# Performance work log

Measured on AMD Instinct MI355X. Metric: run time of the kernel, lower is better.

Reference implementation:

```python
import jax, jax.numpy as jnp
import numpy as np

B, T, C, L, H, OD = 8, 1024, 512, 6, 8, 768
DH = C // H
EPS = 1e-5


def _ln(x, w, b):
    mu = jnp.mean(x, axis=-1, keepdims=True)
    var = jnp.mean((x - mu) ** 2, axis=-1, keepdims=True)
    return (x - mu) * jax.lax.rsqrt(var + EPS) * w + b


def setup_inputs() -> dict:
    key = jax.random.key(0)
    ks = jax.random.split(key, 10)
    s = 0.02
    return {
        "observations": jax.random.normal(ks[0], (B, T, OD), jnp.float32),
        "obs_W": jax.random.normal(ks[1], (OD, C), jnp.float32) * s,
        "obs_b": jnp.zeros((C,), jnp.float32),
        "pos_emb": jax.random.normal(ks[2], (1, T + 1, C), jnp.float32) * s,
        "ln1_w": jnp.ones((L, C), jnp.float32),
        "ln1_b": jnp.zeros((L, C), jnp.float32),
        "Wq": jax.random.normal(ks[3], (L, C, C), jnp.float32) * s,
        "bq": jnp.zeros((L, C), jnp.float32),
        "Wk": jax.random.normal(ks[4], (L, C, C), jnp.float32) * s,
        "bk": jnp.zeros((L, C), jnp.float32),
        "Wv": jax.random.normal(ks[5], (L, C, C), jnp.float32) * s,
        "bv": jnp.zeros((L, C), jnp.float32),
        "Wo": jax.random.normal(ks[6], (L, C, C), jnp.float32) * s,
        "bo": jnp.zeros((L, C), jnp.float32),
        "ln2_w": jnp.ones((L, C), jnp.float32),
        "ln2_b": jnp.zeros((L, C), jnp.float32),
        "W1": jax.random.normal(ks[7], (L, C, 4 * C), jnp.float32) * s,
        "b1": jnp.zeros((L, 4 * C), jnp.float32),
        "W2": jax.random.normal(ks[8], (L, 4 * C, C), jnp.float32) * s,
        "b2": jnp.zeros((L, C), jnp.float32),
        "lnf_w": jnp.ones((C,), jnp.float32),
        "lnf_b": jnp.zeros((C,), jnp.float32),
    }


def reference(observations, obs_W, obs_b, pos_emb, ln1_w, ln1_b, Wq, bq, Wk, bk,
              Wv, bv, Wo, bo, ln2_w, ln2_b, W1, b1, W2, b2, lnf_w, lnf_b):
    # obs embedding: Linear + exact GELU
    tok = jax.nn.gelu(observations @ obs_W + obs_b, approximate=False)
    x = tok + pos_emb[:, :T, :]  # past_length = 0
    causal = jnp.tril(jnp.ones((T, T), bool))  # [T,T]
    scale = 1.0 / np.sqrt(DH)
    for i in range(L):
        h = _ln(x, ln1_w[i], ln1_b[i])
        q = (h @ Wq[i] + bq[i]).reshape(B, T, H, DH)
        k = (h @ Wk[i] + bk[i]).reshape(B, T, H, DH)
        v = (h @ Wv[i] + bv[i]).reshape(B, T, H, DH)
        att = jnp.einsum("bqhd,bkhd->bhqk", q, k) * scale
        att = jnp.where(causal, att, -jnp.inf)
        att = jax.nn.softmax(att, axis=-1)
        y = jnp.einsum("bhqk,bkhd->bqhd", att, v).reshape(B, T, C)
        x = x + y @ Wo[i] + bo[i]
        m = _ln(x, ln2_w[i], ln2_b[i])
        m = jax.nn.gelu(m @ W1[i] + b1[i], approximate=False)
        x = x + m @ W2[i] + b2[i]
    return _ln(x, lnf_w, lnf_b)
```

## Files before the change

kernel.cpp:

```cpp
#include <hip/hip_runtime.h>

#define DEVI __device__ __forceinline__

typedef __attribute__((ext_vector_type(8))) short short8;
typedef __attribute__((ext_vector_type(4))) short sh4;
typedef __attribute__((ext_vector_type(4))) float f32x4;

constexpr int Bn = 8, Tn = 1024, Cn = 512, Hn = 8, DHn = 64, Ln = 6, ODn = 768;
constexpr int Mn = Bn * Tn;
constexpr int SQk = 1536;

DEVI short f2bs(float f) {
  unsigned u = __builtin_bit_cast(unsigned, f);
  unsigned r = (u + 0x7FFFu + ((u >> 16) & 1u)) >> 16;
  return (short)r;
}

DEVI float gelu_f(float v) {
  return 0.5f * v * (1.0f + erff(v * 0.70710678118654752f));
}

DEVI void gload_lds16(const void* gp, void* lp) {
  __builtin_amdgcn_global_load_lds(
      (const __attribute__((address_space(1))) unsigned*)gp,
      (__attribute__((address_space(3))) unsigned*)lp, 16, 0, 0);
}

DEVI short8 ld8(const short* p) {
  sh4 a = *(const sh4*)p;
  sh4 b = *(const sh4*)(p + 4);
  return __builtin_shufflevector(a, b, 0, 1, 2, 3, 4, 5, 6, 7);
}

__global__ __launch_bounds__(256) void wtrans4_kernel(
    const float* __restrict__ Wq, const float* __restrict__ Wk,
    const float* __restrict__ Wv, const float* __restrict__ Wo,
    short* __restrict__ wqkvT, short* __restrict__ woT) {
  const int z = blockIdx.z, i = z >> 2, which = z & 3;
  const size_t WCC = (size_t)Cn * Cn;
  const float* W = (which == 0) ? Wq : (which == 1) ? Wk : (which == 2) ? Wv : Wo;
  W += (size_t)i * WCC;
  short* dst = (which < 3) ? (wqkvT + (size_t)i * 3 * WCC + (size_t)which * WCC)
                           : (woT + (size_t)i * WCC);
  __shared__ float tile[32][33];
  const int tx = threadIdx.x & 31, ty = threadIdx.x >> 5;
  const int k0 = blockIdx.y * 32, n0 = blockIdx.x * 32;
#pragma unroll
  for (int q = 0; q < 4; ++q)
    tile[ty + q * 8][tx] = W[(size_t)(k0 + ty + q * 8) * Cn + n0 + tx];
  __syncthreads();
#pragma unroll
  for (int q = 0; q < 4; ++q)
    dst[(size_t)(n0 + ty + q * 8) * Cn + k0 + tx] = f2bs(tile[tx][ty + q * 8]);
}

__global__ __launch_bounds__(256) void wtransL_kernel(
    const float* __restrict__ W, short* __restrict__ Wt, int K, int N) {
  const int l = blockIdx.z;
  W += (size_t)l * K * N;
  Wt += (size_t)l * K * N;
  __shared__ float tile[32][33];
  const int tx = threadIdx.x & 31, ty = threadIdx.x >> 5;
  const int k0 = blockIdx.y * 32, n0 = blockIdx.x * 32;
#pragma unroll
  for (int q = 0; q < 4; ++q)
    tile[ty + q * 8][tx] = W[(size_t)(k0 + ty + q * 8) * N + n0 + tx];
  __syncthreads();
#pragma unroll
  for (int q = 0; q < 4; ++q)
    Wt[(size_t)(n0 + ty + q * 8) * K + k0 + tx] = f2bs(tile[tx][ty + q * 8]);
}

__global__ __launch_bounds__(256) void bcat_kernel(
    const float* __restrict__ bq, const float* __restrict__ bk,
    const float* __restrict__ bv, float* __restrict__ bqkv) {
  const int i = blockIdx.x * 256 + threadIdx.x;
  const int l = i / 1536, c = i - l * 1536;
  float v = (c < 512) ? bq[l * 512 + c]
                      : (c < 1024) ? bk[l * 512 + c - 512] : bv[l * 512 + c - 1024];
  bqkv[i] = v;
}

__global__ __launch_bounds__(256) void cast_kernel(
    const float* __restrict__ in, short* __restrict__ out) {
  const int i = blockIdx.x * 256 + threadIdx.x;
  out[i] = f2bs(in[i]);
}

template <typename OUTT>
__global__ __launch_bounds__(256) void ln_kernel(
    const float* __restrict__ x, const float* __restrict__ w,
    const float* __restrict__ bb, OUTT* __restrict__ out) {
  const int row = blockIdx.x, tid = threadIdx.x;
  const float* xr = x + (size_t)row * Cn;
  const float v0 = xr[tid], v1 = xr[tid + 256];
  float s = v0 + v1, s2 = v0 * v0 + v1 * v1;
#pragma unroll
  for (int m = 1; m < 64; m <<= 1) {
    s += __shfl_xor(s, m);
    s2 += __shfl_xor(s2, m);
  }
  __shared__ float red[8];
  const int wave = tid >> 6, lane = tid & 63;
  if (lane == 0) { red[wave] = s; red[4 + wave] = s2; }
  __syncthreads();
  s = red[0] + red[1] + red[2] + red[3];
  s2 = red[4] + red[5] + red[6] + red[7];
  const float mu = s * (1.0f / Cn);
  const float var = s2 * (1.0f / Cn) - mu * mu;
  const float rstd = rsqrtf(var + 1e-5f);
  const float o0 = (v0 - mu) * rstd * w[tid] + bb[tid];
  const float o1 = (v1 - mu) * rstd * w[tid + 256] + bb[tid + 256];
  if constexpr (sizeof(OUTT) == 2) {
    out[(size_t)row * Cn + tid] = f2bs(o0);
    out[(size_t)row * Cn + tid + 256] = f2bs(o1);
  } else {
    out[(size_t)row * Cn + tid] = o0;
    out[(size_t)row * Cn + tid + 256] = o1;
  }
}

template <int NP, typename OUTT, bool WRITEX>
__global__ __launch_bounds__(256) void lnred_kernel(
    float* __restrict__ x, const float* __restrict__ part,
    const float* __restrict__ w, const float* __restrict__ bb,
    OUTT* __restrict__ out) {
  const int row = blockIdx.x, tid = threadIdx.x;
  const size_t base = (size_t)row * Cn;
  float v0 = x[base + tid], v1 = x[base + tid + 256];
#pragma unroll
  for (int p = 0; p < NP; ++p) {
    v0 += part[(size_t)p * Mn * Cn + base + tid];
    v1 += part[(size_t)p * Mn * Cn + base + tid + 256];
  }
  if constexpr (WRITEX) {
    x[base + tid] = v0;
    x[base + tid + 256] = v1;
  }
  float s = v0 + v1, s2 = v0 * v0 + v1 * v1;
#pragma unroll
  for (int m = 1; m < 64; m <<= 1) {
    s += __shfl_xor(s, m);
    s2 += __shfl_xor(s2, m);
  }
  __shared__ float red[8];
  const int wave = tid >> 6, lane = tid & 63;
  if (lane == 0) { red[wave] = s; red[4 + wave] = s2; }
  __syncthreads();
  s = red[0] + red[1] + red[2] + red[3];
  s2 = red[4] + red[5] + red[6] + red[7];
  const float mu = s * (1.0f / Cn);
  const float var = s2 * (1.0f / Cn) - mu * mu;
  const float rstd = rsqrtf(var + 1e-5f);
  const float o0 = (v0 - mu) * rstd * w[tid] + bb[tid];
  const float o1 = (v1 - mu) * rstd * w[tid + 256] + bb[tid + 256];
  if constexpr (sizeof(OUTT) == 2) {
    out[base + tid] = f2bs(o0);
    out[base + tid + 256] = f2bs(o1);
  } else {
    out[base + tid] = o0;
    out[base + tid + 256] = o1;
  }
}

template <int EPI, int KS>
__global__ __launch_bounds__(256) void gemm_kernel(
    const short* __restrict__ A, const short* __restrict__ Bt,
    const float* __restrict__ bias, short* __restrict__ outb,
    float* __restrict__ resid, const float* __restrict__ pos, int K, int N) {
  __shared__ __align__(16) short As[128 * 64];
  __shared__ __align__(16) short Bs[128 * 64];
  const int tid = threadIdx.x;
  const int lane = tid & 63;
  const int wave = tid >> 6;
  const int m0 = blockIdx.y * 128;
  const int n0 = blockIdx.x * 128;
  const int z = (KS > 1) ? blockIdx.z : 0;
  const int Ksl = K / KS;
  const int wr = (wave >> 1) * 64;
  const int wc = (wave & 1) * 64;
  const int lA = lane & 15;
  const int lg = lane >> 4;

  f32x4 acc[4][4];
#pragma unroll
  for (int a = 0; a < 4; ++a)
#pragma unroll
    for (int b = 0; b < 4; ++b) acc[a][b] = f32x4{0.f, 0.f, 0.f, 0.f};

  const int rS = tid >> 3;
  const int cS = (((tid & 7) ^ ((tid >> 3) & 7))) * 8;
  const short* Ag = A + (size_t)(m0 + rS) * K + cS;
  const short* Bg = Bt + (size_t)(n0 + rS) * K + cS;

  for (int kk = z * Ksl; kk < z * Ksl + Ksl; kk += 64) {
#pragma unroll
    for (int it = 0; it < 4; ++it) {
      gload_lds16(Ag + (size_t)it * 32 * K + kk, &As[it * 2048 + wave * 512]);
      gload_lds16(Bg + (size_t)it * 32 * K + kk, &Bs[it * 2048 + wave * 512]);
    }
    __syncthreads();
#pragma unroll
    for (int ks = 0; ks < 2; ++ks) {
      const int gA = ((ks * 4 + lg) ^ (lA & 7)) * 8;
      short8 af[4], bf[4];
#pragma unroll
      for (int i = 0; i < 4; ++i) {
        af[i] = *(const short8*)&As[(wr + i * 16 + lA) * 64 + gA];
        bf[i] = *(const short8*)&Bs[(wc + i * 16 + lA) * 64 + gA];
      }
#pragma unroll
      for (int mi = 0; mi < 4; ++mi)
#pragma unroll
        for (int ni = 0; ni < 4; ++ni)
          acc[mi][ni] = __builtin_amdgcn_mfma_f32_16x16x32_bf16(
              af[mi], bf[ni], acc[mi][ni], 0, 0, 0);
    }
    __syncthreads();
  }

#pragma unroll
  for (int mi = 0; mi < 4; ++mi) {
    const int row = m0 + wr + mi * 16 + (lane >> 4) * 4;
#pragma unroll
    for (int ni = 0; ni < 4; ++ni) {
      const int col = n0 + wc + ni * 16 + (lane & 15);
      const float bv = (KS == 1 || z == 0) ? bias[col] : 0.f;
#pragma unroll
      for (int j = 0; j < 4; ++j) {
        const float v = acc[mi][ni][j] + bv;
        const size_t idx = (size_t)(row + j) * N + col;
        if constexpr (EPI == 0) {
          outb[idx] = f2bs(v);
        } else if constexpr (EPI == 1) {
          outb[idx] = f2bs(gelu_f(v));
        } else if constexpr (EPI == 2) {
          resid[idx] = gelu_f(v) + pos[(size_t)((row + j) & (Tn - 1)) * Cn + col];
        } else {
          resid[(size_t)z * Mn * N + idx] = v;
        }
      }
    }
  }
}

__global__ __launch_bounds__(256) void attn_kernel(
    const short* __restrict__ qkv, short* __restrict__ y) {
  __shared__ __align__(16) short Kt[2][64 * 64];
  __shared__ __align__(16) short Vt[2][64 * 68];
  __shared__ __align__(16) short Ps[4][32 * 68];
  const int tid = threadIdx.x, lane = tid & 63, wave = tid >> 6;
  const int qb = blockIdx.x;
  const int bh = blockIdx.y;
  const int b = bh >> 3, h = bh & 7;
  const int qw = qb * 128 + wave * 32;
  const short* qp = qkv + (size_t)b * Tn * SQk + h * DHn;
  const short* kp = qp + 512;
  const short* vp = qp + 1024;
  short* yp = y + (size_t)b * Tn * Cn + h * DHn;
  const int lr = lane & 15, lg = lane >> 4;
  const int kr = lane >> 3;
  const int kg = (lane & 7) ^ kr;

  short8 qf[2][2];
#pragma unroll
  for (int rf = 0; rf < 2; ++rf)
#pragma unroll
    for (int ks = 0; ks < 2; ++ks)
      qf[rf][ks] =
          *(const short8*)(qp + (size_t)(qw + rf * 16 + lr) * SQk + ks * 32 + lg * 8);

  f32x4 o[2][4], mrun[2], lrun[2];
#pragma unroll
  for (int rf = 0; rf < 2; ++rf) {
#pragma unroll
    for (int vf = 0; vf < 4; ++vf) o[rf][vf] = f32x4{0.f, 0.f, 0.f, 0.f};
    mrun[rf] = f32x4{-3e38f, -3e38f, -3e38f, -3e38f};
    lrun[rf] = f32x4{0.f, 0.f, 0.f, 0.f};
  }

  const int ntb = qb * 2 + 2;
  const int ntw = qb * 2 + 1 + (wave >> 1);
  short8 vreg[2];

  gload_lds16(kp + (size_t)(wave * 16 + kr) * SQk + kg * 8, &Kt[0][(wave * 16) * 64]);
  gload_lds16(kp + (size_t)(wave * 16 + 8 + kr) * SQk + kg * 8,
              &Kt[0][(wave * 16 + 8) * 64]);
  vreg[0] = *(const short8*)(vp + (size_t)(wave * 16 + kr) * SQk + (lane & 7) * 8);
  vreg[1] = *(const short8*)(vp + (size_t)(wave * 16 + 8 + kr) * SQk + (lane & 7) * 8);
  asm volatile("s_waitcnt vmcnt(0)" ::: "memory");
#pragma unroll
  for (int l = 0; l < 2; ++l) {
    const int kvl = wave * 16 + l * 8 + kr;
#pragma unroll
    for (int j = 0; j < 8; ++j) Vt[0][((lane & 7) * 8 + j) * 68 + kvl] = vreg[l][j];
  }
  __syncthreads();

  for (int t = 0; t < ntb; ++t) {
    const int bb = t & 1, nx = t + 1;
    if (nx < ntb) {
      const int nb = nx * 64;
      gload_lds16(kp + (size_t)(nb + wave * 16 + kr) * SQk + kg * 8,
                  &Kt[nx & 1][(wave * 16) * 64]);
      gload_lds16(kp + (size_t)(nb + wave * 16 + 8 + kr) * SQk + kg * 8,
                  &Kt[nx & 1][(wave * 16 + 8) * 64]);
      vreg[0] = *(const short8*)(vp + (size_t)(nb + wave * 16 + kr) * SQk + (lane & 7) * 8);
      vreg[1] =
          *(const short8*)(vp + (size_t)(nb + wave * 16 + 8 + kr) * SQk + (lane & 7) * 8);
    }
    if (t < ntw) {
      const int kbase = t * 64;
      f32x4 s[2][4];
#pragma unroll
      for (int rf = 0; rf < 2; ++rf)
#pragma unroll
        for (int cf = 0; cf < 4; ++cf) s[rf][cf] = f32x4{0.f, 0.f, 0.f, 0.f};
#pragma unroll
      for (int ks = 0; ks < 2; ++ks) {
        short8 kf[4];
#pragma unroll
        for (int cf = 0; cf < 4; ++cf)
          kf[cf] = *(const short8*)&Kt[bb][(cf * 16 + lr) * 64 +
                                           (((ks * 4 + lg) ^ (lr & 7))) * 8];
#pragma unroll
        for (int rf = 0; rf < 2; ++rf)
#pragma unroll
          for (int cf = 0; cf < 4; ++cf)
            s[rf][cf] = __builtin_amdgcn_mfma_f32_16x16x32_bf16(
                qf[rf][ks], kf[cf], s[rf][cf], 0, 0, 0);
      }
      short* Pw = Ps[wave];
#pragma unroll
      for (int rf = 0; rf < 2; ++rf) {
        f32x4 tm;
#pragma unroll
        for (int j = 0; j < 4; ++j) {
          const int qrow = qw + rf * 16 + lg * 4 + j;
          float mx = -3e38f;
#pragma unroll
          for (int cf = 0; cf < 4; ++cf) {
            float sv = s[rf][cf][j] * 0.125f;
            if (kbase + cf * 16 + lr > qrow) sv = -1e30f;
            s[rf][cf][j] = sv;
            mx = fmaxf(mx, sv);
          }
          tm[j] = mx;
        }
#pragma unroll
        for (int mm = 1; mm < 16; mm <<= 1)
#pragma unroll
          for (int j = 0; j < 4; ++j) tm[j] = fmaxf(tm[j], __shfl_xor(tm[j], mm));
        f32x4 mnew, corr, ps;
#pragma unroll
        for (int j = 0; j < 4; ++j) {
          mnew[j] = fmaxf(mrun[rf][j], tm[j]);
          corr[j] = __expf(mrun[rf][j] - mnew[j]);
          mrun[rf][j] = mnew[j];
          ps[j] = 0.f;
        }
#pragma unroll
        for (int cf = 0; cf < 4; ++cf)
#pragma unroll
          for (int j = 0; j < 4; ++j) {
            const float p = __expf(s[rf][cf][j] - mnew[j]);
            ps[j] += p;
            Pw[(rf * 16 + lg * 4 + j) * 68 + cf * 16 + lr] = f2bs(p);
          }
#pragma unroll
        for (int mm = 1; mm < 16; mm <<= 1)
#pragma unroll
          for (int j = 0; j < 4; ++j) ps[j] += __shfl_xor(ps[j], mm);
#pragma unroll
        for (int j = 0; j < 4; ++j) lrun[rf][j] = lrun[rf][j] * corr[j] + ps[j];
#pragma unroll
        for (int vf = 0; vf < 4; ++vf)
#pragma unroll
          for (int j = 0; j < 4; ++j) o[rf][vf][j] *= corr[j];
      }
      asm volatile("s_waitcnt lgkmcnt(0)" ::: "memory");
      __builtin_amdgcn_sched_barrier(0);
      short8 pa[2][2], vb[4][2];
#pragma unroll
      for (int rf = 0; rf < 2; ++rf)
#pragma unroll
        for (int k2 = 0; k2 < 2; ++k2)
          pa[rf][k2] = ld8(&Pw[(rf * 16 + lr) * 68 + k2 * 32 + lg * 8]);
#pragma unroll
      for (int vf = 0; vf < 4; ++vf)
#pragma unroll
        for (int k2 = 0; k2 < 2; ++k2)
          vb[vf][k2] = ld8(&Vt[bb][(vf * 16 + lr) * 68 + k2 * 32 + lg * 8]);
#pragma unroll
      for (int rf = 0; rf < 2; ++rf)
#pragma unroll
        for (int vf = 0; vf < 4; ++vf)
#pragma unroll
          for (int k2 = 0; k2 < 2; ++k2)
            o[rf][vf] = __builtin_amdgcn_mfma_f32_16x16x32_bf16(
                pa[rf][k2], vb[vf][k2], o[rf][vf], 0, 0, 0);
    }
    asm volatile("s_waitcnt vmcnt(0)" ::: "memory");
    if (nx < ntb) {
#pragma unroll
      for (int l = 0; l < 2; ++l) {
        const int kvl = wave * 16 + l * 8 + kr;
#pragma unroll
        for (int j = 0; j < 8; ++j)
          Vt[nx & 1][((lane & 7) * 8 + j) * 68 + kvl] = vreg[l][j];
      }
    }
    __syncthreads();
  }

#pragma unroll
  for (int rf = 0; rf < 2; ++rf) {
    f32x4 inv;
#pragma unroll
    for (int j = 0; j < 4; ++j) inv[j] = 1.0f / lrun[rf][j];
#pragma unroll
    for (int vf = 0; vf < 4; ++vf)
#pragma unroll
      for (int j = 0; j < 4; ++j)
        yp[(size_t)(qw + rf * 16 + lg * 4 + j) * Cn + vf * 16 + lr] =
            f2bs(o[rf][vf][j] * inv[j]);
  }
}

extern "C" void kernel_launch(void* const* d_in, const int* in_sizes, int n_in,
                              void* d_out, int out_size, void* d_ws, size_t ws_size,
                              hipStream_t stream) {
  const float* observations = (const float*)d_in[0];
  const float* obs_W = (const float*)d_in[1];
  const float* obs_b = (const float*)d_in[2];
  const float* pos_emb = (const float*)d_in[3];
  const float* ln1_w = (const float*)d_in[4];
  const float* ln1_b = (const float*)d_in[5];
  const float* Wq = (const float*)d_in[6];
  const float* bq = (const float*)d_in[7];
  const float* Wk = (const float*)d_in[8];
  const float* bk = (const float*)d_in[9];
  const float* Wv = (const float*)d_in[10];
  const float* bv = (const float*)d_in[11];
  const float* Wo = (const float*)d_in[12];
  const float* bo = (const float*)d_in[13];
  const float* ln2_w = (const float*)d_in[14];
  const float* ln2_b = (const float*)d_in[15];
  const float* W1 = (const float*)d_in[16];
  const float* b1 = (const float*)d_in[17];
  const float* W2 = (const float*)d_in[18];
  const float* b2 = (const float*)d_in[19];
  const float* lnf_w = (const float*)d_in[20];
  const float* lnf_b = (const float*)d_in[21];
  float* out = (float*)d_out;

  char* ws = (char*)d_ws;
  auto alloc = [&](size_t bytes) -> void* {
    void* p = (void*)ws;
    ws += (bytes + 255) & ~(size_t)255;
    return p;
  };
  const size_t WCC = (size_t)Cn * Cn;
  const size_t WCF = (size_t)Cn * 4 * Cn;

  float* xf = (float*)alloc((size_t)Mn * Cn * 4);
  short* hbf = (short*)alloc((size_t)Mn * Cn * 2);
  short* qkvb = (short*)alloc((size_t)Mn * SQk * 2);
  short* ybf = (short*)alloc((size_t)Mn * Cn * 2);
  short* gbf = (short*)alloc((size_t)Mn * 4 * Cn * 2);
  float* partM = (float*)alloc((size_t)2 * Mn * Cn * 4);
  short* obsbf = (short*)alloc((size_t)Mn * ODn * 2);
  short* obsWt = (short*)alloc((size_t)ODn * Cn * 2);
  short* wqkvT = (short*)alloc((size_t)Ln * 3 * WCC * 2);
  short* woT = (short*)alloc((size_t)Ln * WCC * 2);
  short* w1T = (short*)alloc((size_t)Ln * WCF * 2);
  short* w2T = (short*)alloc((size_t)Ln * WCF * 2);
  float* bqkv = (float*)alloc((size_t)Ln * SQk * 4);
  if ((size_t)(ws - (char*)d_ws) > ws_size) return;
  float* partWo = (float*)gbf;

  wtrans4_kernel<<<dim3(16, 16, 24), 256, 0, stream>>>(Wq, Wk, Wv, Wo, wqkvT, woT);
  wtransL_kernel<<<dim3(16, 24, 1), 256, 0, stream>>>(obs_W, obsWt, ODn, Cn);
  wtransL_kernel<<<dim3(64, 16, 6), 256, 0, stream>>>(W1, w1T, Cn, 4 * Cn);
  wtransL_kernel<<<dim3(16, 64, 6), 256, 0, stream>>>(W2, w2T, 4 * Cn, Cn);
  bcat_kernel<<<(Ln * SQk) / 256, 256, 0, stream>>>(bq, bk, bv, bqkv);
  cast_kernel<<<(Mn * ODn) / 256, 256, 0, stream>>>(observations, obsbf);

  gemm_kernel<2, 1><<<dim3(Cn / 128, Mn / 128), 256, 0, stream>>>(
      obsbf, obsWt, obs_b, nullptr, xf, pos_emb, ODn, Cn);

  ln_kernel<short><<<Mn, 256, 0, stream>>>(xf, ln1_w, ln1_b, hbf);

  for (int i = 0; i < Ln; ++i) {
    gemm_kernel<0, 1><<<dim3(12, 64), 256, 0, stream>>>(
        hbf, wqkvT + i * 3 * WCC, bqkv + i * SQk, qkvb, nullptr, nullptr, Cn, SQk);
    attn_kernel<<<dim3(Tn / 128, Bn * Hn), 256, 0, stream>>>(qkvb, ybf);
    gemm_kernel<4, 2><<<dim3(4, 64, 2), 256, 0, stream>>>(
        ybf, woT + i * WCC, bo + i * Cn, nullptr, partWo, nullptr, Cn, Cn);
    lnred_kernel<2, short, true><<<Mn, 256, 0, stream>>>(
        xf, partWo, ln2_w + i * Cn, ln2_b + i * Cn, hbf);
    gemm_kernel<1, 1><<<dim3(16, 64), 256, 0, stream>>>(
        hbf, w1T + i * WCF, b1 + i * 4 * Cn, gbf, nullptr, nullptr, Cn, 4 * Cn);
    gemm_kernel<4, 2><<<dim3(4, 64, 2), 256, 0, stream>>>(
        gbf, w2T + i * WCF, b2 + i * Cn, nullptr, partM, nullptr, 4 * Cn, Cn);
    if (i < Ln - 1) {
      lnred_kernel<2, short, true><<<Mn, 256, 0, stream>>>(
          xf, partM, ln1_w + (i + 1) * Cn, ln1_b + (i + 1) * Cn, hbf);
    } else {
      lnred_kernel<2, float, false><<<Mn, 256, 0, stream>>>(
          xf, partM, lnf_w, lnf_b, out);
    }
  }
}
```

Before: 1.472 ms.

## Pair complementary causal query tiles per attention block and vectorize input cast

The attention kernel now runs 512 threads per block, and each block handles two query tiles: tile qbp and tile 7-qbp. The two tiles share one K/V stream that runs up to the longer tile's length. This is meant to balance causal work across blocks and to load each K/V tile once for both query tiles, with each wave now loading 8 rows instead of 16. The observation cast kernel also moves to float4 loads and 4-wide bf16 stores. The costs are half as many attention blocks and a larger shared-memory footprint for P, which could lower occupancy.

```diff
diff --git a/kernel.cpp b/kernel.cpp
--- a/kernel.cpp
+++ b/kernel.cpp
@@ -82,9 +82,12 @@
 }
 
 __global__ __launch_bounds__(256) void cast_kernel(
-    const float* __restrict__ in, short* __restrict__ out) {
+    const float4* __restrict__ in, sh4* __restrict__ out) {
   const int i = blockIdx.x * 256 + threadIdx.x;
-  out[i] = f2bs(in[i]);
+  const float4 v = in[i];
+  sh4 o;
+  o[0] = f2bs(v.x); o[1] = f2bs(v.y); o[2] = f2bs(v.z); o[3] = f2bs(v.w);
+  out[i] = o;
 }
 
 template <typename OUTT>
@@ -244,16 +247,18 @@
   }
 }
 
-__global__ __launch_bounds__(256) void attn_kernel(
+__global__ __launch_bounds__(512) void attn_kernel(
     const short* __restrict__ qkv, short* __restrict__ y) {
   __shared__ __align__(16) short Kt[2][64 * 64];
   __shared__ __align__(16) short Vt[2][64 * 68];
-  __shared__ __align__(16) short Ps[4][32 * 68];
+  __shared__ __align__(16) short Ps[8][32 * 68];
   const int tid = threadIdx.x, lane = tid & 63, wave = tid >> 6;
-  const int qb = blockIdx.x;
+  const int qbp = blockIdx.x;
   const int bh = blockIdx.y;
   const int b = bh >> 3, h = bh & 7;
-  const int qw = qb * 128 + wave * 32;
+  const int qtile = (wave < 4) ? qbp : (7 - qbp);
+  const int w4 = wave & 3;
+  const int qw = qtile * 128 + w4 * 32;
   const short* qp = qkv + (size_t)b * Tn * SQk + h * DHn;
   const short* kp = qp + 512;
   const short* vp = qp + 1024;
@@ -279,21 +284,17 @@
     lrun[rf] = f32x4{0.f, 0.f, 0.f, 0.f};
   }
 
-  const int ntb = qb * 2 + 2;
-  const int ntw = qb * 2 + 1 + (wave >> 1);
-  short8 vreg[2];
-
-  gload_lds16(kp + (size_t)(wave * 16 + kr) * SQk + kg * 8, &Kt[0][(wave * 16) * 64]);
-  gload_lds16(kp + (size_t)(wave * 16 + 8 + kr) * SQk + kg * 8,
-              &Kt[0][(wave * 16 + 8) * 64]);
-  vreg[0] = *(const short8*)(vp + (size_t)(wave * 16 + kr) * SQk + (lane & 7) * 8);
-  vreg[1] = *(const short8*)(vp + (size_t)(wave * 16 + 8 + kr) * SQk + (lane & 7) * 8);
+  const int ntb = (7 - qbp) * 2 + 2;
+  const int ntw = qtile * 2 + 1 + (w4 >> 1);
+  short8 vreg;
+
+  gload_lds16(kp + (size_t)(wave * 8 + kr) * SQk + kg * 8, &Kt[0][(wave * 8) * 64]);
+  vreg = *(const short8*)(vp + (size_t)(wave * 8 + kr) * SQk + (lane & 7) * 8);
   asm volatile("s_waitcnt vmcnt(0)" ::: "memory");
-#pragma unroll
-  for (int l = 0; l < 2; ++l) {
-    const int kvl = wave * 16 + l * 8 + kr;
-#pragma unroll
-    for (int j = 0; j < 8; ++j) Vt[0][((lane & 7) * 8 + j) * 68 + kvl] = vreg[l][j];
+  {
+    const int kvl = wave * 8 + kr;
+#pragma unroll
+    for (int j = 0; j < 8; ++j) Vt[0][((lane & 7) * 8 + j) * 68 + kvl] = vreg[j];
   }
   __syncthreads();
 
@@ -301,13 +302,9 @@
     const int bb = t & 1, nx = t + 1;
     if (nx < ntb) {
       const int nb = nx * 64;
-      gload_lds16(kp + (size_t)(nb + wave * 16 + kr) * SQk + kg * 8,
-                  &Kt[nx & 1][(wave * 16) * 64]);
-      gload_lds16(kp + (size_t)(nb + wave * 16 + 8 + kr) * SQk + kg * 8,
-                  &Kt[nx & 1][(wave * 16 + 8) * 64]);
-      vreg[0] = *(const short8*)(vp + (size_t)(nb + wave * 16 + kr) * SQk + (lane & 7) * 8);
-      vreg[1] =
-          *(const short8*)(vp + (size_t)(nb + wave * 16 + 8 + kr) * SQk + (lane & 7) * 8);
+      gload_lds16(kp + (size_t)(nb + wave * 8 + kr) * SQk + kg * 8,
+                  &Kt[nx & 1][(wave * 8) * 64]);
+      vreg = *(const short8*)(vp + (size_t)(nb + wave * 8 + kr) * SQk + (lane & 7) * 8);
     }
     if (t < ntw) {
       const int kbase = t * 64;
@@ -402,13 +399,10 @@
     }
     asm volatile("s_waitcnt vmcnt(0)" ::: "memory");
     if (nx < ntb) {
-#pragma unroll
-      for (int l = 0; l < 2; ++l) {
-        const int kvl = wave * 16 + l * 8 + kr;
-#pragma unroll
-        for (int j = 0; j < 8; ++j)
-          Vt[nx & 1][((lane & 7) * 8 + j) * 68 + kvl] = vreg[l][j];
-      }
+      const int kvl = wave * 8 + kr;
+#pragma unroll
+      for (int j = 0; j < 8; ++j)
+        Vt[nx & 1][((lane & 7) * 8 + j) * 68 + kvl] = vreg[j];
     }
     __syncthreads();
   }
@@ -484,7 +478,8 @@
   wtransL_kernel<<<dim3(64, 16, 6), 256, 0, stream>>>(W1, w1T, Cn, 4 * Cn);
   wtransL_kernel<<<dim3(16, 64, 6), 256, 0, stream>>>(W2, w2T, 4 * Cn, Cn);
   bcat_kernel<<<(Ln * SQk) / 256, 256, 0, stream>>>(bq, bk, bv, bqkv);
-  cast_kernel<<<(Mn * ODn) / 256, 256, 0, stream>>>(observations, obsbf);
+  cast_kernel<<<(Mn * ODn) / 1024, 256, 0, stream>>>(
+      (const float4*)observations, (sh4*)obsbf);
 
   gemm_kernel<2, 1><<<dim3(Cn / 128, Mn / 128), 256, 0, stream>>>(
       obsbf, obsWt, obs_b, nullptr, xf, pos_emb, ODn, Cn);
@@ -494,7 +489,7 @@
   for (int i = 0; i < Ln; ++i) {
     gemm_kernel<0, 1><<<dim3(12, 64), 256, 0, stream>>>(
         hbf, wqkvT + i * 3 * WCC, bqkv + i * SQk, qkvb, nullptr, nullptr, Cn, SQk);
-    attn_kernel<<<dim3(Tn / 128, Bn * Hn), 256, 0, stream>>>(qkvb, ybf);
+    attn_kernel<<<dim3(4, Bn * Hn), 512, 0, stream>>>(qkvb, ybf);
     gemm_kernel<4, 2><<<dim3(4, 64, 2), 256, 0, stream>>>(
         ybf, woT + i * WCC, bo + i * Cn, nullptr, partWo, nullptr, Cn, Cn);
     lnred_kernel<2, short, true><<<Mn, 256, 0, stream>>>(
```

After: 1.369 ms. 1.08x faster.
